# Optimization experiments

Hardware: AMD Instinct MI355X
Metric: run time of the kernel (lower is better)

Reference implementation:

```python
import jax, jax.numpy as jnp
from jax import lax
import numpy as np

SCALE_N = 4
KERN = 5
PAD = KERN // 2
_G = np.float32([[0.003765, 0.015019, 0.023792, 0.015019, 0.003765],
                 [0.015019, 0.059912, 0.094907, 0.059912, 0.015019],
                 [0.023792, 0.094907, 0.150342, 0.094907, 0.023792],
                 [0.015019, 0.059912, 0.094907, 0.059912, 0.015019],
                 [0.003765, 0.015019, 0.023792, 0.015019, 0.003765]])
FILTER = jnp.asarray(_G)


def _lap_split(img):
    N, c, H, W = img.shape
    f = jnp.broadcast_to(FILTER, (c, 1, KERN, KERN))
    smooth = lax.conv_general_dilated(img, f, (1, 1), [(PAD, PAD), (PAD, PAD)],
                                      feature_group_count=c)
    lo = smooth[:, :, ::2, ::2]
    oph, opw = (H + 1) % 2, (W + 1) % 2
    # conv_transpose2d(stride=2, padding=PAD, output_padding) as lhs-dilated conv
    # (Gaussian kernel is symmetric, so no spatial flip needed)
    lo2 = 4.0 * lax.conv_general_dilated(
        lo, f, (1, 1),
        [(KERN - 1 - PAD, KERN - 1 - PAD + oph), (KERN - 1 - PAD, KERN - 1 - PAD + opw)],
        lhs_dilation=(2, 2), feature_group_count=c)
    hi = img - lo2
    return lo, hi


def _pyramid(img):
    levels = []
    for _ in range(SCALE_N):
        img, hi = _lap_split(img)
        levels.append(hi)
    levels.append(img)
    return levels


def _sample_points(img, xs, ys):
    # bilinear grid_sample, align_corners=False, zero padding.
    # img: (N,C,H,W); xs, ys: (P,) normalized coords in [-1,1]. -> (N,C,P)
    N, C, H, W = img.shape
    fx = ((xs + 1.0) * W - 1.0) * 0.5
    fy = ((ys + 1.0) * H - 1.0) * 0.5
    x0 = jnp.floor(fx)
    y0 = jnp.floor(fy)
    wx = fx - x0
    wy = fy - y0
    x0i = x0.astype(jnp.int32)
    y0i = y0.astype(jnp.int32)
    out = jnp.zeros((N, C, xs.shape[0]), img.dtype)
    corners = [(0, 0, (1 - wx) * (1 - wy)), (1, 0, wx * (1 - wy)),
               (0, 1, (1 - wx) * wy), (1, 1, wx * wy)]
    for dx, dy, w in corners:
        xc = x0i + dx
        yc = y0i + dy
        valid = (xc >= 0) & (xc < W) & (yc >= 0) & (yc < H)
        xcc = jnp.clip(xc, 0, W - 1)
        ycc = jnp.clip(yc, 0, H - 1)
        vals = img[:, :, ycc, xcc]  # (N,C,P) gather
        out = out + vals * (w * valid)[None, None, :]
    return out


def setup_inputs() -> dict:
    key = jax.random.key(0)
    k1, k2, k3 = jax.random.split(key, 3)
    N, c, H, W = 64, 32, 128, 128
    outdims = 4096
    m = SCALE_N + 1
    x = jax.random.normal(k1, (N, c, H, W), dtype=jnp.float32)
    grid = jax.random.uniform(k2, (1, outdims, 1, 2), minval=-0.1, maxval=0.1,
                              dtype=jnp.float32)
    features = (jnp.full((1, m * c, 1, outdims), 1.0 / c, jnp.float32)
                + 0.01 * jax.random.normal(k3, (1, m * c, 1, outdims), jnp.float32))
    bias = jnp.zeros((outdims,), jnp.float32)
    return {"x": x, "grid": grid, "features": features, "bias": bias}


def reference(x, grid, features, bias):
    N, c, H, W = x.shape
    m = SCALE_N + 1
    outdims = grid.shape[1]
    g = jnp.clip(grid, -1.0, 1.0)
    xs = g[0, :, 0, 0]  # width coord
    ys = g[0, :, 0, 1]  # height coord
    levels = _pyramid(x)
    pools = [_sample_points(lv, xs, ys) for lv in levels]  # each (N,c,P)
    y = jnp.concatenate(pools, axis=1)  # (N, m*c, P)
    feat = features.reshape(1, m * c, outdims)
    y = (y * feat).sum(axis=1)  # (N, P)
    return y + bias
```

## Files before the change

### kernel.cpp

```cpp
#include <hip/hip_runtime.h>
#include <hip/hip_fp16.h>


#define P1 66
#define P2 34
#define P3 18
#define P4 10
#define OFF_LO1 0
#define OFF_LO2 4224
#define OFF_LO3 5312
#define OFF_LO4 5600
#define SLOT    5680
#define SLOT4   1420

#define G_A 0.0613609f
#define G_B 0.2447700f
#define G_C 0.3877386f

#define T_FOFF   16384
#define PYR_FOFF 196608
#define PSTRIDE  5696

static __device__ __forceinline__ float clampf(float v, float lo, float hi) {
    return fminf(fmaxf(v, lo), hi);
}
static __device__ __forceinline__ int imin(int a, int b) { return a < b ? a : b; }
static __device__ __forceinline__ int imax(int a, int b) { return a > b ? a : b; }

static __device__ __forceinline__ unsigned int pack_h2(float a, float b) {
    __half ha = __float2half_rn(a), hb = __float2half_rn(b);
    unsigned short ua = *(unsigned short*)&ha, ub = *(unsigned short*)&hb;
    return (unsigned int)ua | ((unsigned int)ub << 16);
}
static __device__ __forceinline__ unsigned int pack_u2(int a, int b) {
    return (unsigned int)(a & 0xffff) | ((unsigned int)b << 16);
}
static __device__ __forceinline__ float2 uph2(unsigned int u) {
    unsigned short lo = (unsigned short)(u & 0xffff), hi = (unsigned short)(u >> 16);
    __half hl = *(__half*)&lo, hh = *(__half*)&hi;
    return make_float2(__half2float(hl), __half2float(hh));
}

__global__ void init_out_kernel(const float* __restrict__ bias, float* __restrict__ y) {
    int i = blockIdx.x * blockDim.x + threadIdx.x;
    y[i] = bias[i & 4095];
}

__global__ void weights_kernel(const float* __restrict__ grid, float* __restrict__ ws) {
    int out = blockIdx.x * blockDim.x + threadIdx.x;
    if (out >= 4096) return;
    float xs = clampf(grid[2 * out + 0], -1.f, 1.f);
    float ys = clampf(grid[2 * out + 1], -1.f, 1.f);

    uint4* L0 = (uint4*)ws;
    uint2* T  = (uint2*)(ws + T_FOFF);

    float fx = (xs + 1.f) * 64.f - 0.5f;
    float fy = (ys + 1.f) * 64.f - 0.5f;
    float x0f = floorf(fx), y0f = floorf(fy);
    int x0 = (int)x0f, y0 = (int)y0f;
    float wx = fx - x0f, wy = fy - y0f;
    float ux0 = (x0 >= 0)      ? (1.f - wx) : 0.f;
    float ux1 = (x0 + 1 < 128) ? wx         : 0.f;
    float uy0 = (y0 >= 0)      ? (1.f - wy) : 0.f;
    float uy1 = (y0 + 1 < 128) ? wy         : 0.f;
    int cx0 = imax(x0, 0), cx1 = imin(x0 + 1, 127);
    int cy0 = imax(y0, 0), cy1 = imin(y0 + 1, 127);
    L0[out] = make_uint4(pack_h2(ux0 * uy0, ux1 * uy0),
                         pack_h2(ux0 * uy1, ux1 * uy1),
                         pack_u2(cy0 * 128 + cx0, cy0 * 128 + cx1),
                         pack_u2(cy1 * 128 + cx0, cy1 * 128 + cx1));

    int   x0p = x0, y0p = y0;
    float ux0p = ux0, ux1p = ux1, uy0p = uy0, uy1p = uy1;

    const int offs[4]    = {OFF_LO1, OFF_LO2, OFF_LO3, OFF_LO4};
    const int strides[4] = {P1, P2, P3, P4};

    for (int j = 1; j <= 4; ++j) {
        const int Wj = 128 >> j, Pj = strides[j - 1], off = offs[j - 1];

        int qx; float a0, a1, a2;
        if (x0p & 1) { qx = (x0p - 1) >> 1;
            a0 = G_B * ux0p + G_A * ux1p; a1 = G_B * ux0p + G_C * ux1p; a2 = G_A * ux1p; }
        else         { qx = (x0p >> 1) - 1;
            a0 = G_A * ux0p; a1 = G_C * ux0p + G_B * ux1p; a2 = G_A * ux0p + G_B * ux1p; }
        int qy; float e0, e1, e2;
        if (y0p & 1) { qy = (y0p - 1) >> 1;
            e0 = G_B * uy0p + G_A * uy1p; e1 = G_B * uy0p + G_C * uy1p; e2 = G_A * uy1p; }
        else         { qy = (y0p >> 1) - 1;
            e0 = G_A * uy0p; e1 = G_C * uy0p + G_B * uy1p; e2 = G_A * uy0p + G_B * uy1p; }

        float half = (float)(Wj >> 1);
        float fxj = (xs + 1.f) * half - 0.5f;
        float fyj = (ys + 1.f) * half - 0.5f;
        float x0jf = floorf(fxj), y0jf = floorf(fyj);
        int x0j = (int)x0jf, y0j = (int)y0jf;
        float wxj = fxj - x0jf, wyj = fyj - y0jf;
        float ux0j = (x0j >= 0)     ? (1.f - wxj) : 0.f;
        float ux1j = (x0j + 1 < Wj) ? wxj         : 0.f;
        float uy0j = (y0j >= 0)     ? (1.f - wyj) : 0.f;
        float uy1j = (y0j + 1 < Wj) ? wyj         : 0.f;

        int bxb = qx & ~1;
        bxb = imin(imax(bxb, 0), Wj - 4);

        float axv[4], bxv[4], ayv[3], byv[3];
        int rv[3];
#pragma unroll
        for (int t = 0; t < 4; ++t) {
            int col = bxb + t;
            int s = col - qx;
            float av = (s == 0) ? a0 : (s == 1) ? a1 : (s == 2) ? a2 : 0.f;
            if (s < 0 || s > 2) av = 0.f;
            int sb = col - x0j;
            float bv = (sb == 0) ? ux0j : (sb == 1) ? ux1j : 0.f;
            axv[t] = av;
            bxv[t] = bv;
        }
#pragma unroll
        for (int t = 0; t < 3; ++t) {
            int row = qy + t;
            bool v = (row >= 0) && (row < Wj);
            float av = (t == 0) ? e0 : (t == 1) ? e1 : e2;
            ayv[t] = v ? av : 0.f;
            int sb = row - y0j;
            byv[t] = (sb == 0) ? uy0j : (sb == 1) ? uy1j : 0.f;
            int rc = imin(imax(row, 0), Wj - 1);
            rv[t] = off + rc * Pj + bxb;
        }

        int tb = (j - 1) * 5 * 4096 + out;
        T[tb]            = make_uint2(pack_h2(axv[0], axv[1]), pack_h2(axv[2], axv[3]));
        T[tb + 4096]     = make_uint2(pack_h2(bxv[0], bxv[1]), pack_h2(bxv[2], bxv[3]));
        T[tb + 2 * 4096] = make_uint2(pack_h2(ayv[0], ayv[1]), pack_h2(ayv[2], 0.f));
        T[tb + 3 * 4096] = make_uint2(pack_h2(byv[0], byv[1]), pack_h2(byv[2], 0.f));
        T[tb + 4 * 4096] = make_uint2(pack_u2(rv[0], rv[1]), pack_u2(rv[2], 0));

        x0p = x0j; y0p = y0j;
        ux0p = ux0j; ux1p = ux1j; uy0p = uy0j; uy1p = uy1j;
    }
}

static __device__ __forceinline__ float down_pt_lds(const float* s, int stride, int S,
                                                    int i, int j) {
    const float g1[5] = {G_A, G_B, G_C, G_B, G_A};
    int by = 2 * i - 2, bx = 2 * j - 2;
    float acc = 0.f;
    if (by >= 0 && by + 4 < S && bx >= 0 && bx + 4 < S) {
#pragma unroll
        for (int dy = 0; dy < 5; ++dy) {
            const float* r = s + (by + dy) * stride + bx;
            acc += g1[dy] * (G_A * (r[0] + r[4]) + G_B * (r[1] + r[3]) + G_C * r[2]);
        }
    } else {
#pragma unroll
        for (int dy = 0; dy < 5; ++dy) {
            int yy = by + dy;
            if ((unsigned)yy < (unsigned)S) {
#pragma unroll
                for (int dx = 0; dx < 5; ++dx) {
                    int xx = bx + dx;
                    if ((unsigned)xx < (unsigned)S)
                        acc += g1[dy] * g1[dx] * s[yy * stride + xx];
                }
            }
        }
    }
    return acc;
}

static __device__ __forceinline__ void border_quad(const float* __restrict__ img,
                                                   int i, int j0, float acc[4]) {
    const float g1[5] = {G_A, G_B, G_C, G_B, G_A};
    int by = 2 * i - 2, bx = 2 * j0 - 2;
#pragma unroll
    for (int dy = 0; dy < 5; ++dy) {
        int yy = by + dy;
        if ((unsigned)yy < 128u) {
#pragma unroll
            for (int t = 0; t < 11; ++t) {
                int xx = bx + t;
                if ((unsigned)xx < 128u) {
                    float v = img[yy * 128 + xx];
#pragma unroll
                    for (int jj = 0; jj < 4; ++jj) {
                        int dx = t - 2 * jj;
                        if (dx >= 0 && dx <= 4) acc[jj] += g1[dy] * g1[dx] * v;
                    }
                }
            }
        }
    }
}

static __device__ __forceinline__ void build_pyramid1(const float* __restrict__ img,
                                                      float* __restrict__ s_lo, int tid) {
    const float g1[5] = {G_A, G_B, G_C, G_B, G_A};

    {
        const int jq = tid & 15;
        const int s  = tid >> 4;
        const int j0 = jq << 2;
        float acc[4][4] = {{0.f,0.f,0.f,0.f},{0.f,0.f,0.f,0.f},
                           {0.f,0.f,0.f,0.f},{0.f,0.f,0.f,0.f}};
        if (jq >= 1 && jq <= 14) {
            const int a = 2 * j0 - 4;
            const int ybase = 8 * s - 2;
#pragma unroll
            for (int t5 = 0; t5 < 11; ++t5) {
                int y = ybase + t5;
                if ((unsigned)y < 128u) {
                    const float* rp = img + y * 128 + a;
                    float4 q0 = *(const float4*)(rp);
                    float4 q1 = *(const float4*)(rp + 4);
                    float4 q2 = *(const float4*)(rp + 8);
                    float4 q3 = *(const float4*)(rp + 12);
                    float s2 = q0.z, s3 = q0.w, s4 = q1.x, s5 = q1.y, s6 = q1.z,
                          s7 = q1.w, s8 = q2.x, s9 = q2.y, s10 = q2.z, s11 = q2.w,
                          s12 = q3.x;
                    float h0 = G_A * (s2 + s6)  + G_B * (s3 + s5)  + G_C * s4;
                    float h1 = G_A * (s4 + s8)  + G_B * (s5 + s7)  + G_C * s6;
                    float h2 = G_A * (s6 + s10) + G_B * (s7 + s9)  + G_C * s8;
                    float h3 = G_A * (s8 + s12) + G_B * (s9 + s11) + G_C * s10;
#pragma unroll
                    for (int k = 0; k < 4; ++k) {
                        int dy = t5 - 2 * k;
                        if (dy >= 0 && dy <= 4) {
                            float g = g1[dy];
                            acc[k][0] += g * h0; acc[k][1] += g * h1;
                            acc[k][2] += g * h2; acc[k][3] += g * h3;
                        }
                    }
                }
            }
        } else {
#pragma unroll
            for (int k = 0; k < 4; ++k)
                border_quad(img, 4 * s + k, j0, acc[k]);
        }
#pragma unroll
        for (int k = 0; k < 4; ++k) {
            int base = OFF_LO1 + (4 * s + k) * P1 + j0;
            *(float2*)&s_lo[base]     = make_float2(acc[k][0], acc[k][1]);
            *(float2*)&s_lo[base + 2] = make_float2(acc[k][2], acc[k][3]);
        }
    }
    __syncthreads();

    for (int p = tid; p < 1024; p += 256) {
        int i = p >> 5, j = p & 31;
        s_lo[OFF_LO2 + i * P2 + j] = down_pt_lds(s_lo + OFF_LO1, P1, 64, i, j);
    }
    __syncthreads();

    {
        int i = tid >> 4, j = tid & 15;
        s_lo[OFF_LO3 + i * P3 + j] = down_pt_lds(s_lo + OFF_LO2, P2, 32, i, j);
    }
    __syncthreads();

    if (tid < 64) {
        int i = tid >> 3, j = tid & 7;
        s_lo[OFF_LO4 + i * P4 + j] = down_pt_lds(s_lo + OFF_LO3, P3, 16, i, j);
    }
    __syncthreads();
}

__global__ __launch_bounds__(256) void pyr_build_kernel(
    const float* __restrict__ x, float* __restrict__ ws)
{
    __shared__ __align__(16) float s_lo[SLOT];
    const int tid = threadIdx.x;
    const int bid = blockIdx.x;
    const float* img = x + ((size_t)bid << 14);

    build_pyramid1(img, s_lo, tid);

    float4* g4 = (float4*)(ws + PYR_FOFF + (size_t)bid * PSTRIDE);
    const float4* s4 = (const float4*)s_lo;
    for (int i = tid; i < SLOT4; i += 256) g4[i] = s4[i];
}

__global__ __launch_bounds__(256) void pyr_gather_kernel(
    const float* __restrict__ x, const float* __restrict__ wrec,
    const float* __restrict__ feat, const float* __restrict__ bias,
    float* __restrict__ y)
{
    __shared__ __align__(16) float s_p[2][PSTRIDE];
    const int tid  = threadIdx.x;
    const int bid  = blockIdx.x;
    const int sw   = ((bid & 7) << 7) | (bid >> 3);
    const int n    = sw >> 4;
    const int tile = sw & 15;
    const int out  = (tile << 8) + tid;

    const uint4* L0 = (const uint4*)wrec;
    const uint2* T  = (const uint2*)(wrec + T_FOFF);

    uint4 h0 = L0[out];
    float2 wA = uph2(h0.x), wB = uph2(h0.y);
    int o00 = (int)(h0.z & 0xffff), o01 = (int)(h0.z >> 16);
    int o10 = (int)(h0.w & 0xffff), o11 = (int)(h0.w >> 16);

    float ax[4][4], bx[4][4], ay[4][3], by[4][3];
    int   rv[4][3];
#pragma unroll
    for (int j = 0; j < 4; ++j) {
        const int tb = j * 5 * 4096 + out;
        uint2 uAX = T[tb];
        uint2 uBX = T[tb + 4096];
        uint2 uAY = T[tb + 2 * 4096];
        uint2 uBY = T[tb + 3 * 4096];
        uint2 uR  = T[tb + 4 * 4096];
        float2 t;
        t = uph2(uAX.x); ax[j][0] = t.x; ax[j][1] = t.y;
        t = uph2(uAX.y); ax[j][2] = t.x; ax[j][3] = t.y;
        t = uph2(uBX.x); bx[j][0] = t.x; bx[j][1] = t.y;
        t = uph2(uBX.y); bx[j][2] = t.x; bx[j][3] = t.y;
        t = uph2(uAY.x); ay[j][0] = t.x; ay[j][1] = t.y;
        ay[j][2] = uph2(uAY.y).x;
        t = uph2(uBY.x); by[j][0] = t.x; by[j][1] = t.y;
        by[j][2] = uph2(uBY.y).x;
        rv[j][0] = (int)(uR.x & 0xffff);
        rv[j][1] = (int)(uR.x >> 16);
        rv[j][2] = (int)(uR.y & 0xffff);
    }

    const float* img_n = x + ((size_t)n << 19);
    const float* pyr_n = wrec + PYR_FOFF + (size_t)n * 32 * PSTRIDE;

    {
        const float4* g = (const float4*)pyr_n;
        float4* d = (float4*)s_p[0];
        for (int i = tid; i < SLOT4; i += 256) d[i] = g[i];
    }
    __syncthreads();

    float acc = 0.f;
#pragma unroll 1
    for (int c = 0; c < 32; ++c) {
        const int cur = c & 1;

        float4 st0, st1, st2, st3, st4, st5;
        const bool have_next = (c + 1 < 32);
        if (have_next) {
            const float4* g = (const float4*)(pyr_n + (size_t)(c + 1) * PSTRIDE);
            int i0 = tid;
            st0 = g[i0];
            st1 = g[i0 + 256];
            st2 = g[i0 + 512];
            st3 = g[i0 + 768];
            st4 = g[i0 + 1024];
            st5 = (i0 + 1280 < SLOT4) ? g[i0 + 1280] : make_float4(0.f, 0.f, 0.f, 0.f);
        }

        const float* sl  = s_p[cur];
        const float* img = img_n + ((size_t)c << 14);
        float f_prev = feat[((size_t)c << 12) + out];
        float v0 = wA.x * img[o00] + wA.y * img[o01] + wB.x * img[o10] + wB.y * img[o11];
        float a = f_prev * v0;

#pragma unroll
        for (int j = 0; j < 4; ++j) {
            float f_cur = feat[((size_t)((j + 1) * 32 + c) << 12) + out];
            int r0 = rv[j][0], r1 = rv[j][1], r2 = rv[j][2];
            float2 p0a = *(const float2*)(sl + r0);
            float2 p0b = *(const float2*)(sl + r0 + 2);
            float2 p1a = *(const float2*)(sl + r1);
            float2 p1b = *(const float2*)(sl + r1 + 2);
            float2 p2a = *(const float2*)(sl + r2);
            float2 p2b = *(const float2*)(sl + r2 + 2);
            float ra0 = ax[j][0] * p0a.x + ax[j][1] * p0a.y + ax[j][2] * p0b.x + ax[j][3] * p0b.y;
            float ra1 = ax[j][0] * p1a.x + ax[j][1] * p1a.y + ax[j][2] * p1b.x + ax[j][3] * p1b.y;
            float ra2 = ax[j][0] * p2a.x + ax[j][1] * p2a.y + ax[j][2] * p2b.x + ax[j][3] * p2b.y;
            float rb0 = bx[j][0] * p0a.x + bx[j][1] * p0a.y + bx[j][2] * p0b.x + bx[j][3] * p0b.y;
            float rb1 = bx[j][0] * p1a.x + bx[j][1] * p1a.y + bx[j][2] * p1b.x + bx[j][3] * p1b.y;
            float rb2 = bx[j][0] * p2a.x + bx[j][1] * p2a.y + bx[j][2] * p2b.x + bx[j][3] * p2b.y;
            float sa = ay[j][0] * ra0 + ay[j][1] * ra1 + ay[j][2] * ra2;
            float sb = by[j][0] * rb0 + by[j][1] * rb1 + by[j][2] * rb2;
            a += f_cur * sb - 4.f * f_prev * sa;
            f_prev = f_cur;
        }
        acc += a;

        if (have_next) {
            float4* d = (float4*)s_p[cur ^ 1];
            int i0 = tid;
            d[i0]        = st0;
            d[i0 + 256]  = st1;
            d[i0 + 512]  = st2;
            d[i0 + 768]  = st3;
            d[i0 + 1024] = st4;
            if (i0 + 1280 < SLOT4) d[i0 + 1280] = st5;
        }
        __syncthreads();
    }

    y[((size_t)n << 12) + out] = acc + bias[out];
}

__global__ __launch_bounds__(256, 3) void pyr_sample_fused(
    const float* __restrict__ x, const float* __restrict__ wrec,
    const float* __restrict__ feat, float* __restrict__ y)
{
    __shared__ __align__(16) float s_lo[SLOT];
    const int tid = threadIdx.x;
    const int n   = blockIdx.x >> 5;
    const int c   = blockIdx.x & 31;
    const float* img = x + ((size_t)(n * 32 + c) << 14);

    build_pyramid1(img, s_lo, tid);

    const uint4* L0 = (const uint4*)wrec;
    const uint2* T  = (const uint2*)(wrec + T_FOFF);
    float* yrow = y + ((size_t)n << 12);
    for (int out = tid; out < 4096; out += 256) {
        uint4 h0 = L0[out];
        float2 wA = uph2(h0.x), wB = uph2(h0.y);
        int o00 = (int)(h0.z & 0xffff), o01 = (int)(h0.z >> 16);
        int o10 = (int)(h0.w & 0xffff), o11 = (int)(h0.w >> 16);

        float f_prev = feat[((size_t)c << 12) + out];
        float v0 = wA.x * img[o00] + wA.y * img[o01] + wB.x * img[o10] + wB.y * img[o11];
        float acc = f_prev * v0;

#pragma unroll
        for (int j = 1; j <= 4; ++j) {
            const int tb = (j - 1) * 5 * 4096 + out;
            uint2 uAX = T[tb];
            uint2 uBX = T[tb + 4096];
            uint2 uAY = T[tb + 2 * 4096];
            uint2 uBY = T[tb + 3 * 4096];
            uint2 uR  = T[tb + 4 * 4096];
            float2 ax01 = uph2(uAX.x), ax23 = uph2(uAX.y);
            float2 bx01 = uph2(uBX.x), bx23 = uph2(uBX.y);
            float2 ay01 = uph2(uAY.x); float ay2 = uph2(uAY.y).x;
            float2 by01 = uph2(uBY.x); float by2 = uph2(uBY.y).x;
            int r0 = (int)(uR.x & 0xffff), r1 = (int)(uR.x >> 16), r2 = (int)(uR.y & 0xffff);

            float f_cur = feat[((size_t)(j * 32 + c) << 12) + out];

            float2 p0a = *(const float2*)&s_lo[r0];
            float2 p0b = *(const float2*)&s_lo[r0 + 2];
            float2 p1a = *(const float2*)&s_lo[r1];
            float2 p1b = *(const float2*)&s_lo[r1 + 2];
            float2 p2a = *(const float2*)&s_lo[r2];
            float2 p2b = *(const float2*)&s_lo[r2 + 2];
            float ra0 = ax01.x * p0a.x + ax01.y * p0a.y + ax23.x * p0b.x + ax23.y * p0b.y;
            float ra1 = ax01.x * p1a.x + ax01.y * p1a.y + ax23.x * p1b.x + ax23.y * p1b.y;
            float ra2 = ax01.x * p2a.x + ax01.y * p2a.y + ax23.x * p2b.x + ax23.y * p2b.y;
            float rb0 = bx01.x * p0a.x + bx01.y * p0a.y + bx23.x * p0b.x + bx23.y * p0b.y;
            float rb1 = bx01.x * p1a.x + bx01.y * p1a.y + bx23.x * p1b.x + bx23.y * p1b.y;
            float rb2 = bx01.x * p2a.x + bx01.y * p2a.y + bx23.x * p2b.x + bx23.y * p2b.y;
            float sa = ay01.x * ra0 + ay01.y * ra1 + ay2 * ra2;
            float sb = by01.x * rb0 + by01.y * rb1 + by2 * rb2;
            acc += f_cur * sb - 4.f * f_prev * sa;
            f_prev = f_cur;
        }
        atomicAdd(&yrow[out], acc);
    }
}

extern "C" void kernel_launch(void* const* d_in, const int* in_sizes, int n_in,
                              void* d_out, int out_size, void* d_ws, size_t ws_size,
                              hipStream_t stream) {
    (void)in_sizes; (void)n_in;
    const float* x    = (const float*)d_in[0];
    const float* grid = (const float*)d_in[1];
    const float* feat = (const float*)d_in[2];
    const float* bias = (const float*)d_in[3];
    float* y  = (float*)d_out;
    float* ws = (float*)d_ws;

    const size_t NEED = sizeof(float) * ((size_t)PYR_FOFF + 2048ull * PSTRIDE);

    weights_kernel<<<16, 256, 0, stream>>>(grid, ws);
    if (ws_size >= NEED) {
        pyr_build_kernel<<<2048, 256, 0, stream>>>(x, ws);
        pyr_gather_kernel<<<1024, 256, 0, stream>>>(x, ws, feat, bias, y);
    } else {
        init_out_kernel<<<out_size / 256, 256, 0, stream>>>(bias, y);
        pyr_sample_fused<<<2048, 256, 0, stream>>>(x, ws, feat, y);
    }
}
```

Baseline: 344.7 us.

## Split pyramid build into separate lo1 and downsample kernels

The pyramid build kernel is split in two. The first kernel computes the level-1 lowpass with no shared memory and writes it straight to the workspace with float4 stores. The second kernel reloads that level into LDS, builds the coarser levels and writes back only the new tail. The LDS row pitch for level 1 shrinks from 66 to 64, which shrinks the workspace stride. The aim is to raise occupancy for the memory-bound first pass, at the cost of an extra launch and an extra global round trip for level 1, plus possible LDS bank conflicts at the new pitch.

```diff
diff --git a/kernel.cpp b/kernel.cpp
--- a/kernel.cpp
+++ b/kernel.cpp
@@ -2,16 +2,16 @@
 #include <hip/hip_fp16.h>
 
 
-#define P1 66
+#define P1 64
 #define P2 34
 #define P3 18
 #define P4 10
 #define OFF_LO1 0
-#define OFF_LO2 4224
-#define OFF_LO3 5312
-#define OFF_LO4 5600
-#define SLOT    5680
-#define SLOT4   1420
+#define OFF_LO2 4096
+#define OFF_LO3 5184
+#define OFF_LO4 5472
+#define SLOT    5552
+#define SLOT4   1388
 
 #define G_A 0.0613609f
 #define G_B 0.2447700f
@@ -19,7 +19,7 @@
 
 #define T_FOFF   16384
 #define PYR_FOFF 196608
-#define PSTRIDE  5696
+#define PSTRIDE  5568
 
 static __device__ __forceinline__ float clampf(float v, float lo, float hi) {
     return fminf(fmaxf(v, lo), hi);
@@ -194,92 +194,117 @@
     }
 }
 
-static __device__ __forceinline__ void build_pyramid1(const float* __restrict__ img,
-                                                      float* __restrict__ s_lo, int tid) {
+static __device__ __forceinline__ void hconv4(const float* __restrict__ rp,
+                                              float h[4]) {
+    float4 q0 = *(const float4*)(rp);
+    float4 q1 = *(const float4*)(rp + 4);
+    float4 q2 = *(const float4*)(rp + 8);
+    float4 q3 = *(const float4*)(rp + 12);
+    float s2 = q0.z, s3 = q0.w, s4 = q1.x, s5 = q1.y, s6 = q1.z,
+          s7 = q1.w, s8 = q2.x, s9 = q2.y, s10 = q2.z, s11 = q2.w,
+          s12 = q3.x;
+    h[0] = G_A * (s2 + s6)  + G_B * (s3 + s5)  + G_C * s4;
+    h[1] = G_A * (s4 + s8)  + G_B * (s5 + s7)  + G_C * s6;
+    h[2] = G_A * (s6 + s10) + G_B * (s7 + s9)  + G_C * s8;
+    h[3] = G_A * (s8 + s12) + G_B * (s9 + s11) + G_C * s10;
+}
+
+static __device__ __forceinline__ void lo1_strip(const float* __restrict__ img,
+                                                 int s, int jq, float acc[4][4]) {
     const float g1[5] = {G_A, G_B, G_C, G_B, G_A};
-
-    {
-        const int jq = tid & 15;
-        const int s  = tid >> 4;
-        const int j0 = jq << 2;
-        float acc[4][4] = {{0.f,0.f,0.f,0.f},{0.f,0.f,0.f,0.f},
-                           {0.f,0.f,0.f,0.f},{0.f,0.f,0.f,0.f}};
-        if (jq >= 1 && jq <= 14) {
-            const int a = 2 * j0 - 4;
-            const int ybase = 8 * s - 2;
-#pragma unroll
-            for (int t5 = 0; t5 < 11; ++t5) {
-                int y = ybase + t5;
-                if ((unsigned)y < 128u) {
-                    const float* rp = img + y * 128 + a;
-                    float4 q0 = *(const float4*)(rp);
-                    float4 q1 = *(const float4*)(rp + 4);
-                    float4 q2 = *(const float4*)(rp + 8);
-                    float4 q3 = *(const float4*)(rp + 12);
-                    float s2 = q0.z, s3 = q0.w, s4 = q1.x, s5 = q1.y, s6 = q1.z,
-                          s7 = q1.w, s8 = q2.x, s9 = q2.y, s10 = q2.z, s11 = q2.w,
-                          s12 = q3.x;
-                    float h0 = G_A * (s2 + s6)  + G_B * (s3 + s5)  + G_C * s4;
-                    float h1 = G_A * (s4 + s8)  + G_B * (s5 + s7)  + G_C * s6;
-                    float h2 = G_A * (s6 + s10) + G_B * (s7 + s9)  + G_C * s8;
-                    float h3 = G_A * (s8 + s12) + G_B * (s9 + s11) + G_C * s10;
-#pragma unroll
-                    for (int k = 0; k < 4; ++k) {
-                        int dy = t5 - 2 * k;
-                        if (dy >= 0 && dy <= 4) {
-                            float g = g1[dy];
-                            acc[k][0] += g * h0; acc[k][1] += g * h1;
-                            acc[k][2] += g * h2; acc[k][3] += g * h3;
-                        }
+    const int j0 = jq << 2;
+#pragma unroll
+    for (int k = 0; k < 4; ++k)
+#pragma unroll
+        for (int t = 0; t < 4; ++t) acc[k][t] = 0.f;
+    if (jq >= 1 && jq <= 14) {
+        const int a = 2 * j0 - 4;
+        const int ybase = 8 * s - 2;
+#pragma unroll
+        for (int t5 = 0; t5 < 11; ++t5) {
+            int y = ybase + t5;
+            if ((unsigned)y < 128u) {
+                float h[4];
+                hconv4(img + y * 128 + a, h);
+#pragma unroll
+                for (int k = 0; k < 4; ++k) {
+                    int dy = t5 - 2 * k;
+                    if (dy >= 0 && dy <= 4) {
+                        float g = g1[dy];
+                        acc[k][0] += g * h[0]; acc[k][1] += g * h[1];
+                        acc[k][2] += g * h[2]; acc[k][3] += g * h[3];
                     }
                 }
             }
-        } else {
-#pragma unroll
-            for (int k = 0; k < 4; ++k)
-                border_quad(img, 4 * s + k, j0, acc[k]);
-        }
-#pragma unroll
-        for (int k = 0; k < 4; ++k) {
-            int base = OFF_LO1 + (4 * s + k) * P1 + j0;
-            *(float2*)&s_lo[base]     = make_float2(acc[k][0], acc[k][1]);
-            *(float2*)&s_lo[base + 2] = make_float2(acc[k][2], acc[k][3]);
-        }
-    }
-    __syncthreads();
-
-    for (int p = tid; p < 1024; p += 256) {
-        int i = p >> 5, j = p & 31;
-        s_lo[OFF_LO2 + i * P2 + j] = down_pt_lds(s_lo + OFF_LO1, P1, 64, i, j);
-    }
-    __syncthreads();
-
-    {
-        int i = tid >> 4, j = tid & 15;
-        s_lo[OFF_LO3 + i * P3 + j] = down_pt_lds(s_lo + OFF_LO2, P2, 32, i, j);
-    }
-    __syncthreads();
-
-    if (tid < 64) {
-        int i = tid >> 3, j = tid & 7;
-        s_lo[OFF_LO4 + i * P4 + j] = down_pt_lds(s_lo + OFF_LO3, P3, 16, i, j);
-    }
-    __syncthreads();
-}
-
-__global__ __launch_bounds__(256) void pyr_build_kernel(
+        }
+    } else {
+#pragma unroll
+        for (int k = 0; k < 4; ++k)
+            border_quad(img, 4 * s + k, j0, acc[k]);
+    }
+}
+
+__global__ __launch_bounds__(256) void pyr_lo1_kernel(
     const float* __restrict__ x, float* __restrict__ ws)
+{
+    const int tid = threadIdx.x;
+    const int bid = blockIdx.x;
+    const float* img = x + ((size_t)bid << 14);
+    float* slot = ws + PYR_FOFF + (size_t)bid * PSTRIDE;
+
+    const int jq = tid & 15, s = tid >> 4;
+    float acc[4][4];
+    lo1_strip(img, s, jq, acc);
+
+    const int j0 = jq << 2;
+#pragma unroll
+    for (int k = 0; k < 4; ++k) {
+        *(float4*)(slot + (4 * s + k) * P1 + j0) =
+            make_float4(acc[k][0], acc[k][1], acc[k][2], acc[k][3]);
+    }
+}
+
+__global__ __launch_bounds__(256) void pyr_down_kernel(float* __restrict__ ws)
 {
     __shared__ __align__(16) float s_lo[SLOT];
     const int tid = threadIdx.x;
     const int bid = blockIdx.x;
-    const float* img = x + ((size_t)bid << 14);
-
-    build_pyramid1(img, s_lo, tid);
-
-    float4* g4 = (float4*)(ws + PYR_FOFF + (size_t)bid * PSTRIDE);
-    const float4* s4 = (const float4*)s_lo;
-    for (int i = tid; i < SLOT4; i += 256) g4[i] = s4[i];
+    float* slot = ws + PYR_FOFF + (size_t)bid * PSTRIDE;
+
+    {
+        const float4* g = (const float4*)slot;
+        float4* d = (float4*)s_lo;
+#pragma unroll
+        for (int i = 0; i < 4; ++i) d[tid + 256 * i] = g[tid + 256 * i];
+    }
+    __syncthreads();
+
+    for (int p = tid; p < 1024; p += 256) {
+        int i = p >> 5, j = p & 31;
+        s_lo[OFF_LO2 + i * P2 + j] = down_pt_lds(s_lo + OFF_LO1, P1, 64, i, j);
+    }
+    __syncthreads();
+
+    {
+        int i = tid >> 4, j = tid & 15;
+        s_lo[OFF_LO3 + i * P3 + j] = down_pt_lds(s_lo + OFF_LO2, P2, 32, i, j);
+    }
+    __syncthreads();
+
+    if (tid < 64) {
+        int i = tid >> 3, j = tid & 7;
+        s_lo[OFF_LO4 + i * P4 + j] = down_pt_lds(s_lo + OFF_LO3, P3, 16, i, j);
+    }
+    __syncthreads();
+
+    {
+        float4* g = (float4*)slot;
+        const float4* d = (const float4*)s_lo;
+        int i = 1024 + tid;
+        if (i < SLOT4) g[i] = d[i];
+        i += 256;
+        if (i < SLOT4) g[i] = d[i];
+    }
 }
 
 __global__ __launch_bounds__(256) void pyr_gather_kernel(
@@ -400,6 +425,38 @@
     y[((size_t)n << 12) + out] = acc + bias[out];
 }
 
+static __device__ __forceinline__ void build_pyramid1(const float* __restrict__ img,
+                                                      float* __restrict__ s_lo, int tid) {
+    {
+        const int jq = tid & 15, s = tid >> 4;
+        float acc[4][4];
+        lo1_strip(img, s, jq, acc);
+        const int j0 = jq << 2;
+#pragma unroll
+        for (int k = 0; k < 4; ++k) {
+            int base = OFF_LO1 + (4 * s + k) * P1 + j0;
+            *(float4*)&s_lo[base] =
+                make_float4(acc[k][0], acc[k][1], acc[k][2], acc[k][3]);
+        }
+    }
+    __syncthreads();
+    for (int p = tid; p < 1024; p += 256) {
+        int i = p >> 5, j = p & 31;
+        s_lo[OFF_LO2 + i * P2 + j] = down_pt_lds(s_lo + OFF_LO1, P1, 64, i, j);
+    }
+    __syncthreads();
+    {
+        int i = tid >> 4, j = tid & 15;
+        s_lo[OFF_LO3 + i * P3 + j] = down_pt_lds(s_lo + OFF_LO2, P2, 32, i, j);
+    }
+    __syncthreads();
+    if (tid < 64) {
+        int i = tid >> 3, j = tid & 7;
+        s_lo[OFF_LO4 + i * P4 + j] = down_pt_lds(s_lo + OFF_LO3, P3, 16, i, j);
+    }
+    __syncthreads();
+}
+
 __global__ __launch_bounds__(256, 3) void pyr_sample_fused(
     const float* __restrict__ x, const float* __restrict__ wrec,
     const float* __restrict__ feat, float* __restrict__ y)
@@ -477,7 +534,8 @@
 
     weights_kernel<<<16, 256, 0, stream>>>(grid, ws);
     if (ws_size >= NEED) {
-        pyr_build_kernel<<<2048, 256, 0, stream>>>(x, ws);
+        pyr_lo1_kernel<<<2048, 256, 0, stream>>>(x, ws);
+        pyr_down_kernel<<<2048, 256, 0, stream>>>(ws);
         pyr_gather_kernel<<<1024, 256, 0, stream>>>(x, ws, feat, bias, y);
     } else {
         init_out_kernel<<<out_size / 256, 256, 0, stream>>>(bias, y);
```

Result: slower. 359.4 us (+4.3%).
